# Kernel optimization log

Measured on AMD Instinct MI355X. Metric: run time of the kernel, lower is better.

The kernel has to match this reference:

```python
import jax, jax.numpy as jnp
import numpy as np

N = 50000          # total nodes
N_USER = 40000     # main (user) nodes
E = 400000         # edges per node kind
K = 3              # node kinds (separate graphs)
H = 4              # attention heads
F_IN = 128         # n_units[0]
F_OUT = 64         # n_units[1]
NB_CLASSES = 40
SLOPE = 0.2        # leaky relu negative slope


def setup_inputs() -> dict:
    key = jax.random.key(0)
    ks = jax.random.split(key, 12)
    h = jax.random.normal(ks[0], (N, F_IN), dtype=jnp.float32)
    edge_index = jax.random.randint(ks[1], (K, 2, E), 0, N, dtype=jnp.int32)
    # per-kind SpGATLayer params (bias=False)
    w = jax.random.normal(ks[2], (K, H, F_IN, F_OUT), dtype=jnp.float32) * 0.1
    a_src = jax.random.normal(ks[3], (K, H, F_OUT), dtype=jnp.float32) * 0.1
    a_trg = jax.random.normal(ks[4], (K, H, F_OUT), dtype=jnp.float32) * 0.1
    # AdditiveAttention: w1 (d=F_IN -> d2=F_OUT), w2 (d1=F_OUT -> d2=F_OUT), m (d2 -> 1)
    w1 = jax.random.normal(ks[5], (F_IN, F_OUT), dtype=jnp.float32) * 0.1
    w2 = jax.random.normal(ks[6], (F_OUT, F_OUT), dtype=jnp.float32) * 0.1
    m = jax.random.normal(ks[7], (F_OUT,), dtype=jnp.float32) * 0.1
    # final fc: in = F_OUT*(K+1)
    fc_w = jax.random.normal(ks[8], (F_OUT * (K + 1), NB_CLASSES), dtype=jnp.float32) * 0.1
    fc_b = jnp.zeros((NB_CLASSES,), dtype=jnp.float32)
    return {"h": h, "edge_index": edge_index, "w": w, "a_src": a_src,
            "a_trg": a_trg, "w1": w1, "w2": w2, "m": m,
            "fc_w": fc_w, "fc_b": fc_b}


def _spgat_kind(h, src, trg, wk, ask, atk):
    # h: [N, F_IN], wk: [H, F_IN, F_OUT], ask/atk: [H, F_OUT]
    hp = jnp.einsum('nd,hdf->nhf', h, wk)               # [N, H, F_OUT]
    s = jnp.einsum('nhf,hf->nh', hp, ask)               # [N, H]
    t = jnp.einsum('nhf,hf->nh', hp, atk)               # [N, H]
    e = s[src] + t[trg]                                 # [E, H]
    e = jnp.where(e >= 0, e, SLOPE * e)                 # leaky relu
    e = e - jnp.max(e)                                  # global max shift (as in source)
    exp_e = jnp.exp(e)
    denom = jax.ops.segment_sum(exp_e, trg, num_segments=N)  # [N, H]
    alpha = exp_e / (denom[trg] + 1e-16)                # [E, H]
    msg = hp[src] * alpha[:, :, None]                   # [E, H, F_OUT]
    out = jax.ops.segment_sum(msg, trg, num_segments=N) # [N, H, F_OUT]
    return out.mean(axis=1)                             # [N, F_OUT] (last layer head-mean)


def reference(h, edge_index, w, a_src, a_trg, w1, w2, m, fc_w, fc_b):
    heter = []
    for k in range(K):  # fixed small loop over node kinds
        x = _spgat_kind(h, edge_index[k, 0], edge_index[k, 1],
                        w[k], a_src[k], a_trg[k])
        heter.append(x[:N_USER])
    type_aware = jnp.stack(heter, axis=1)               # [N_USER, K, F_OUT]
    feature = h[:N_USER]                                # [N_USER, F_IN]
    q = jnp.tanh((feature @ w1)[:, None, :] + type_aware @ w2)  # [N_USER, K, F_OUT]
    scores = q @ m                                      # [N_USER, K]
    beta = jax.nn.softmax(scores, axis=-1)
    fusion = jnp.einsum('nk,nkf->nf', beta, type_aware) # [N_USER, F_OUT]
    ret = jnp.concatenate([type_aware, fusion[:, None, :]], axis=1)
    ret = ret.reshape(N_USER, -1)                       # [N_USER, F_OUT*(K+1)]
    logits = ret @ fc_w + fc_b
    return jax.nn.log_softmax(logits, axis=-1)
```

## Files before the change

### kernel.cpp

```cpp
#include <hip/hip_runtime.h>
#include <hip/hip_bf16.h>

#define NN    50000
#define NUSER 40000
#define EE    400000
#define KKIND 3
#define HHEAD 4
#define FIN   128
#define FOUT  64
#define NCLS  40

typedef __attribute__((ext_vector_type(8))) short short8;
typedef __attribute__((ext_vector_type(4))) float floatx4;

__device__ __forceinline__ float bf2f(unsigned short u) {
    unsigned int v = ((unsigned int)u) << 16;
    return __uint_as_float(v);
}
__device__ __forceinline__ unsigned short f2bf(float f) {
    unsigned int u = __float_as_uint(f);
    unsigned int r = (u + 0x7FFFu + ((u >> 16) & 1u)) >> 16;
    return (unsigned short)r;
}

#define OFF_H    0
#define OFF_W    6400000
#define OFF_ASRC 6498304
#define OFF_ATRG 6499072
#define OFF_W1   6499840
#define OFF_W2   6508032
#define OFF_M    6512128
#define OFF_FCW  6512192
#define OFF_FCB  6522432
#define CONV_TOT 6522472

__global__ __launch_bounds__(256) void detect_kernel(const unsigned short* __restrict__ hraw,
                                                     int* __restrict__ flag)
{
    __shared__ int cnt;
    if (threadIdx.x == 0) cnt = 0;
    __syncthreads();
    int local = 0;
#pragma unroll
    for (int j = 0; j < 8; j++) {
        unsigned short u = hraw[threadIdx.x * 8 + j];
        int ex = (u >> 7) & 0xFF;
        if (ex >= 0x90) local++;
    }
    atomicAdd(&cnt, local);
    __syncthreads();
    if (threadIdx.x == 0) *flag = (cnt > 100) ? 1 : 0;
}

__global__ __launch_bounds__(256) void conv_kernel(const void* __restrict__ p0, const void* __restrict__ p2,
                                                   const void* __restrict__ p3, const void* __restrict__ p4,
                                                   const void* __restrict__ p5, const void* __restrict__ p6,
                                                   const void* __restrict__ p7, const void* __restrict__ p8,
                                                   const void* __restrict__ p9,
                                                   const int* __restrict__ flagp,
                                                   unsigned short* __restrict__ dst)
{
    int tid = (blockIdx.x * 256 + threadIdx.x) * 8;
    if (tid >= CONV_TOT) return;
    const void* src; int li;
    if      (tid < OFF_W)    { src = p0; li = tid - OFF_H; }
    else if (tid < OFF_ASRC) { src = p2; li = tid - OFF_W; }
    else if (tid < OFF_ATRG) { src = p3; li = tid - OFF_ASRC; }
    else if (tid < OFF_W1)   { src = p4; li = tid - OFF_ATRG; }
    else if (tid < OFF_W2)   { src = p5; li = tid - OFF_W1; }
    else if (tid < OFF_M)    { src = p6; li = tid - OFF_W2; }
    else if (tid < OFF_FCW)  { src = p7; li = tid - OFF_M; }
    else if (tid < OFF_FCB)  { src = p8; li = tid - OFF_FCW; }
    else                     { src = p9; li = tid - OFF_FCB; }
    if (*flagp) {
        const float* fp = (const float*)src + li;
        float4 x = *(const float4*)fp;
        float4 y = *(const float4*)(fp + 4);
        uint4 o;
        o.x = (unsigned int)f2bf(x.x) | ((unsigned int)f2bf(x.y) << 16);
        o.y = (unsigned int)f2bf(x.z) | ((unsigned int)f2bf(x.w) << 16);
        o.z = (unsigned int)f2bf(y.x) | ((unsigned int)f2bf(y.y) << 16);
        o.w = (unsigned int)f2bf(y.z) | ((unsigned int)f2bf(y.w) << 16);
        *(uint4*)(dst + tid) = o;
    } else {
        *(uint4*)(dst + tid) = *(const uint4*)((const unsigned short*)src + li);
    }
}

__global__ __launch_bounds__(256) void repack_w(const unsigned short* __restrict__ w,
                                                unsigned short* __restrict__ wT)
{
    int tid = blockIdx.x * 256 + threadIdx.x;
    if (tid >= 12288) return;
    int f = tid & 63, g = (tid >> 6) & 15, h = (tid >> 10) & 3, k = tid >> 12;
    const unsigned short* src = w + (size_t)(k * 4 + h) * 8192 + f;
    unsigned short* dst = wT + (size_t)tid * 8;
#pragma unroll
    for (int j = 0; j < 8; j++) dst[j] = src[(size_t)(g * 8 + j) * 64];
}

__global__ __launch_bounds__(256) void repack_small(const unsigned short* __restrict__ w1,
                                                    const unsigned short* __restrict__ w2,
                                                    const unsigned short* __restrict__ fcw,
                                                    unsigned short* __restrict__ w1T,
                                                    unsigned short* __restrict__ w2T,
                                                    unsigned short* __restrict__ fcwT)
{
    int tid = blockIdx.x * 256 + threadIdx.x;
    if (tid < 1024) {
        int c = tid & 63, g = tid >> 6;
#pragma unroll
        for (int j = 0; j < 8; j++) w1T[(size_t)(g * 64 + c) * 8 + j] = w1[(size_t)(g * 8 + j) * 64 + c];
    } else if (tid < 1536) {
        int t = tid - 1024; int c = t & 63, g = t >> 6;
#pragma unroll
        for (int j = 0; j < 8; j++) w2T[(size_t)(g * 64 + c) * 8 + j] = w2[(size_t)(g * 8 + j) * 64 + c];
    } else if (tid < 3072) {
        int t = tid - 1536; int c = t % 48, g = t / 48;
#pragma unroll
        for (int j = 0; j < 8; j++)
            fcwT[(size_t)(g * 48 + c) * 8 + j] = (c < NCLS) ? fcw[(size_t)(g * 8 + j) * NCLS + c] : (unsigned short)0;
    }
}

__global__ __launch_bounds__(256) void hist3(const int* __restrict__ ei,
                                             unsigned int* __restrict__ cnt,
                                             unsigned int* __restrict__ rank)
{
    int k = blockIdx.y;
    const int* trg = ei + (size_t)k * 2 * EE + EE;
    unsigned int* ck = cnt + (size_t)k * NUSER;
    unsigned int* rk = rank + (size_t)k * EE;
    int e0 = blockIdx.x * 1024 + threadIdx.x;
    int t[4];
#pragma unroll
    for (int j = 0; j < 4; j++) {
        int e = e0 + j * 256;
        t[j] = (e < EE) ? trg[e] : NUSER;
    }
    unsigned int r[4];
#pragma unroll
    for (int j = 0; j < 4; j++)
        r[j] = (t[j] < NUSER) ? atomicAdd(&ck[t[j]], 1u) : 0u;
#pragma unroll
    for (int j = 0; j < 4; j++) {
        int e = e0 + j * 256;
        if (e < EE && t[j] < NUSER) rk[e] = r[j];
    }
}

#define SCB 20
__global__ __launch_bounds__(256) void scanA(const unsigned int* __restrict__ cnt,
                                             unsigned int* __restrict__ partials)
{
    int k = blockIdx.y, b = blockIdx.x;
    const unsigned int* c = cnt + (size_t)k * NUSER;
    int base = b * 2048 + threadIdx.x * 8;
    unsigned int s = 0;
#pragma unroll
    for (int j = 0; j < 8; j++) { int idx = base + j; if (idx < NUSER) s += c[idx]; }
#pragma unroll
    for (int off = 1; off < 64; off <<= 1) s += __shfl_xor(s, off, 64);
    __shared__ unsigned int wsum[4];
    int lane = threadIdx.x & 63, wid = threadIdx.x >> 6;
    if (lane == 0) wsum[wid] = s;
    __syncthreads();
    if (threadIdx.x == 0) partials[k * SCB + b] = wsum[0] + wsum[1] + wsum[2] + wsum[3];
}

__global__ __launch_bounds__(256) void scanB(unsigned int* __restrict__ partials,
                                             unsigned int* __restrict__ rowptr)
{
    int wid = threadIdx.x >> 6, lane = threadIdx.x & 63;
    if (wid >= KKIND) return;
    unsigned int v = (lane < SCB) ? partials[wid * SCB + lane] : 0u;
    unsigned int inc = v;
#pragma unroll
    for (int off = 1; off < 32; off <<= 1) {
        unsigned int u = __shfl_up(inc, off, 64);
        if (lane >= off) inc += u;
    }
    if (lane < SCB) partials[wid * SCB + lane] = inc - v;
    if (lane == SCB - 1) rowptr[(size_t)wid * (NUSER + 1) + NUSER] = inc;
}

__global__ __launch_bounds__(256) void scanC(const unsigned int* __restrict__ cnt,
                                             const unsigned int* __restrict__ partials,
                                             unsigned int* __restrict__ rowptr)
{
    int k = blockIdx.y, b = blockIdx.x;
    const unsigned int* c = cnt + (size_t)k * NUSER;
    unsigned int* rp = rowptr + (size_t)k * (NUSER + 1);
    int lane = threadIdx.x & 63, wid = threadIdx.x >> 6;
    int base = b * 2048 + threadIdx.x * 8;
    unsigned int vals[8]; unsigned int s = 0;
#pragma unroll
    for (int j = 0; j < 8; j++) { int idx = base + j; vals[j] = (idx < NUSER) ? c[idx] : 0u; s += vals[j]; }
    unsigned int inc = s;
#pragma unroll
    for (int off = 1; off < 64; off <<= 1) {
        unsigned int u = __shfl_up(inc, off, 64);
        if (lane >= off) inc += u;
    }
    __shared__ unsigned int wsum[4];
    if (lane == 63) wsum[wid] = inc;
    __syncthreads();
    unsigned int woff = 0;
    for (int i = 0; i < wid; i++) woff += wsum[i];
    unsigned int run = partials[k * SCB + b] + woff + (inc - s);
#pragma unroll
    for (int j = 0; j < 8; j++) {
        int idx = base + j;
        if (idx < NUSER) { rp[idx] = run; run += vals[j]; }
    }
}

__global__ __launch_bounds__(256) void scatter3(const int* __restrict__ ei,
                                                const unsigned int* __restrict__ rowptr,
                                                const unsigned int* __restrict__ rank,
                                                int* __restrict__ srcl)
{
    int k = blockIdx.y;
    const int* srcA = ei + (size_t)k * 2 * EE;
    const int* trg = srcA + EE;
    const unsigned int* rp = rowptr + (size_t)k * (NUSER + 1);
    const unsigned int* rk = rank + (size_t)k * EE;
    int* sl = srcl + (size_t)k * EE;
    int e0 = blockIdx.x * 1024 + threadIdx.x;
    int t[4], s[4]; unsigned int r[4];
#pragma unroll
    for (int j = 0; j < 4; j++) {
        int e = e0 + j * 256;
        t[j] = (e < EE) ? trg[e] : NUSER;
        s[j] = (e < EE) ? srcA[e] : 0;
        r[j] = (e < EE && t[j] < NUSER) ? rk[e] : 0u;
    }
    unsigned int base[4];
#pragma unroll
    for (int j = 0; j < 4; j++) base[j] = (t[j] < NUSER) ? rp[t[j]] : 0u;
#pragma unroll
    for (int j = 0; j < 4; j++) {
        int e = e0 + j * 256;
        if (e < EE && t[j] < NUSER) sl[base[j] + r[j]] = s[j];
    }
}

__global__ __launch_bounds__(256) void hp_gemm_multi(const unsigned short* __restrict__ h,
                                                     const unsigned short* __restrict__ wTall,
                                                     const unsigned short* __restrict__ asrc_all,
                                                     const unsigned short* __restrict__ atrg_all,
                                                     unsigned short* __restrict__ hp2,
                                                     long long hp2_stride,
                                                     float* __restrict__ sb, float* __restrict__ tb,
                                                     int kbeg, int kcnt)
{
    int wave = (blockIdx.x * 256 + threadIdx.x) >> 6;
    int lane = threadIdx.x & 63;
    if (wave >= NN / 16) return;
    int m0 = wave * 16;
    int mi = lane & 15, quad = lane >> 4;

    short8 a[4];
    const unsigned short* hrow = h + (size_t)(m0 + mi) * FIN + quad * 8;
#pragma unroll
    for (int kk = 0; kk < 4; kk++) a[kk] = *(const short8*)(hrow + kk * 32);

    for (int kq = 0; kq < kcnt; kq++) {
        int k = kbeg + kq;
        const unsigned short* wTk = wTall + (size_t)k * 32768;
        const unsigned short* ak_src = asrc_all + k * 256;
        const unsigned short* ak_trg = atrg_all + k * 256;
        unsigned short* hp2k = hp2 + (size_t)kq * hp2_stride;
        float* sbk = sb + (size_t)k * NN * 4;
        float* tbk = tb + (size_t)k * NN * 4;

        float sp[4][4], tp[4][4];
#pragma unroll
        for (int r = 0; r < 4; r++)
#pragma unroll
            for (int q2 = 0; q2 < 4; q2++) { sp[r][q2] = 0.f; tp[r][q2] = 0.f; }

#pragma unroll
        for (int j = 0; j < 4; j++) {
            int fc = j * 16 + mi;
            floatx4 acc4[4];
#pragma unroll
            for (int hh = 0; hh < 4; hh++) {
                floatx4 acc = {0.f, 0.f, 0.f, 0.f};
#pragma unroll
                for (int kk = 0; kk < 4; kk++) {
                    short8 b = *(const short8*)(wTk + (size_t)((hh * 16 + kk * 4 + quad) * 64 + fc) * 8);
                    acc = __builtin_amdgcn_mfma_f32_16x16x32_bf16(a[kk], b, acc, 0, 0, 0);
                }
                acc4[hh] = acc;
                float asv = bf2f(ak_src[hh * 64 + fc]);
                float atv = bf2f(ak_trg[hh * 64 + fc]);
#pragma unroll
                for (int reg = 0; reg < 4; reg++) {
                    sp[reg][hh] += acc[reg] * asv;
                    tp[reg][hh] += acc[reg] * atv;
                }
            }
#pragma unroll
            for (int reg = 0; reg < 4; reg++) {
                ushort4 pk;
                pk.x = f2bf(acc4[0][reg]); pk.y = f2bf(acc4[1][reg]);
                pk.z = f2bf(acc4[2][reg]); pk.w = f2bf(acc4[3][reg]);
                int row = m0 + quad * 4 + reg;
                *(ushort4*)(hp2k + (size_t)row * 256 + fc * 4) = pk;
            }
        }
#pragma unroll
        for (int off = 1; off < 16; off <<= 1)
#pragma unroll
            for (int r = 0; r < 4; r++)
#pragma unroll
                for (int q2 = 0; q2 < 4; q2++) {
                    sp[r][q2] += __shfl_xor(sp[r][q2], off, 64);
                    tp[r][q2] += __shfl_xor(tp[r][q2], off, 64);
                }
        float sv = 0.f, tv = 0.f;
#pragma unroll
        for (int r = 0; r < 4; r++)
#pragma unroll
            for (int q2 = 0; q2 < 4; q2++) {
                bool sel = (mi == r * 4 + q2);
                sv = sel ? sp[r][q2] : sv;
                tv = sel ? tp[r][q2] : tv;
            }
        int rr = m0 + quad * 4 + (mi >> 2);
        sbk[rr * 4 + (mi & 3)] = sv;
        tbk[rr * 4 + (mi & 3)] = tv;
    }
}

__global__ __launch_bounds__(256) void passB_multi(const unsigned int* __restrict__ rowptr_all,
                                                   const int* __restrict__ srcl_all,
                                                   const float* __restrict__ sb,
                                                   const float* __restrict__ tb,
                                                   const unsigned short* __restrict__ hp2,
                                                   long long hp2_stride,
                                                   unsigned short* __restrict__ ret, int kbeg)
{
    __shared__ int    lds_src[4][64];
    __shared__ float4 lds_ew[4][64];
    int kq = blockIdx.y, k = kbeg + kq;
    const unsigned int* rowptr = rowptr_all + (size_t)k * (NUSER + 1);
    const int* srcl = srcl_all + (size_t)k * EE;
    const float* sbk = sb + (size_t)k * NN * 4;
    const float* tbk = tb + (size_t)k * NN * 4;
    const unsigned short* hp2k = hp2 + (size_t)kq * hp2_stride;

    int wid = threadIdx.x >> 6;
    int n = __builtin_amdgcn_readfirstlane(blockIdx.x * 4 + wid);
    int f = threadIdx.x & 63;
    unsigned int beg = rowptr[n], end = rowptr[n + 1];
    float4 t4 = *(const float4*)(tbk + (size_t)n * 4);
    float num0 = 0.f, num1 = 0.f, num2 = 0.f, num3 = 0.f;
    float den0 = 0.f, den1 = 0.f, den2 = 0.f, den3 = 0.f;

    for (unsigned int p0 = beg; p0 < end; p0 += 64) {
        unsigned int cnt = end - p0; if (cnt > 64) cnt = 64;
        int s = 0;
        float4 e = {0.f, 0.f, 0.f, 0.f};
        if ((unsigned int)f < cnt) {
            s = srcl[p0 + f];
            float4 sv = *(const float4*)(sbk + (size_t)s * 4);
            float v0 = sv.x + t4.x, v1 = sv.y + t4.y, v2 = sv.z + t4.z, v3 = sv.w + t4.w;
            v0 = (v0 >= 0.f) ? v0 : 0.2f * v0;  v1 = (v1 >= 0.f) ? v1 : 0.2f * v1;
            v2 = (v2 >= 0.f) ? v2 : 0.2f * v2;  v3 = (v3 >= 0.f) ? v3 : 0.2f * v3;
            e.x = __expf(v0); e.y = __expf(v1); e.z = __expf(v2); e.w = __expf(v3);
        }
        lds_src[wid][f] = s;
        lds_ew[wid][f] = e;
        float d0 = e.x, d1 = e.y, d2 = e.z, d3 = e.w;
#pragma unroll
        for (int off = 1; off < 64; off <<= 1) {
            d0 += __shfl_xor(d0, off, 64); d1 += __shfl_xor(d1, off, 64);
            d2 += __shfl_xor(d2, off, 64); d3 += __shfl_xor(d3, off, 64);
        }
        den0 += d0; den1 += d1; den2 += d2; den3 += d3;
        unsigned int jmax = (cnt + 7u) & ~7u;
        for (unsigned int j = 0; j < jmax; j += 8) {
            int ss[8]; float4 ee[8];
#pragma unroll
            for (int u = 0; u < 8; u++) { ss[u] = lds_src[wid][j + u]; ee[u] = lds_ew[wid][j + u]; }
            ushort4 hv[8];
#pragma unroll
            for (int u = 0; u < 8; u++) hv[u] = *(const ushort4*)(hp2k + (size_t)ss[u] * 256 + f * 4);
#pragma unroll
            for (int u = 0; u < 8; u++) {
                num0 += ee[u].x * bf2f(hv[u].x); num1 += ee[u].y * bf2f(hv[u].y);
                num2 += ee[u].z * bf2f(hv[u].z); num3 += ee[u].w * bf2f(hv[u].w);
            }
        }
    }
    float r = 0.25f * (num0 / (den0 + 1e-16f) + num1 / (den1 + 1e-16f)
                     + num2 / (den2 + 1e-16f) + num3 / (den3 + 1e-16f));
    ret[(size_t)n * 256 + k * 64 + f] = f2bf(r);
}

__global__ __launch_bounds__(256) void qscore2f(const unsigned short* __restrict__ h,
                                                const unsigned short* __restrict__ w1T,
                                                const unsigned short* __restrict__ retA,
                                                const unsigned short* __restrict__ w2T,
                                                const unsigned short* __restrict__ mvec,
                                                unsigned short* __restrict__ ret, int M)
{
    int wave = (blockIdx.x * 256 + threadIdx.x) >> 6;
    int lane = threadIdx.x & 63;
    int m0 = wave * 16;
    if (m0 >= M) return;
    int mi = lane & 15, quad = lane >> 4;

    floatx4 fw[4];
#pragma unroll
    for (int nt = 0; nt < 4; nt++) fw[nt] = (floatx4){0.f, 0.f, 0.f, 0.f};
#pragma unroll
    for (int kk = 0; kk < 4; kk++) {
        short8 a = *(const short8*)(h + (size_t)(m0 + mi) * FIN + kk * 32 + quad * 8);
#pragma unroll
        for (int nt = 0; nt < 4; nt++) {
            short8 b = *(const short8*)(w1T + (size_t)((kk * 4 + quad) * 64 + nt * 16 + mi) * 8);
            fw[nt] = __builtin_amdgcn_mfma_f32_16x16x32_bf16(a, b, fw[nt], 0, 0, 0);
        }
    }

    float pk[3][4];
    short8 afr[3][2];
    for (int k = 0; k < KKIND; k++) {
        floatx4 acc[4];
#pragma unroll
        for (int nt = 0; nt < 4; nt++) acc[nt] = (floatx4){0.f, 0.f, 0.f, 0.f};
#pragma unroll
        for (int kk = 0; kk < 2; kk++) {
            short8 a = *(const short8*)(retA + (size_t)(m0 + mi) * 256 + k * 64 + kk * 32 + quad * 8);
            afr[k][kk] = a;
#pragma unroll
            for (int nt = 0; nt < 4; nt++) {
                short8 b = *(const short8*)(w2T + (size_t)((kk * 4 + quad) * 64 + nt * 16 + mi) * 8);
                acc[nt] = __builtin_amdgcn_mfma_f32_16x16x32_bf16(a, b, acc[nt], 0, 0, 0);
            }
        }
        float part[4] = {0.f, 0.f, 0.f, 0.f};
#pragma unroll
        for (int nt = 0; nt < 4; nt++) {
            int col = nt * 16 + mi;
            float mval = bf2f(mvec[col]);
#pragma unroll
            for (int reg = 0; reg < 4; reg++) {
                float x = acc[nt][reg] + fw[nt][reg];
                float q = 1.f - 2.f / (1.f + __expf(2.f * x));
                part[reg] += q * mval;
            }
        }
#pragma unroll
        for (int off = 1; off < 16; off <<= 1)
#pragma unroll
            for (int reg = 0; reg < 4; reg++) part[reg] += __shfl_xor(part[reg], off, 64);
#pragma unroll
        for (int reg = 0; reg < 4; reg++) pk[k][reg] = part[reg];
    }

    int rsel = mi & 3;
    float sv0 = (rsel == 0) ? pk[0][0] : (rsel == 1) ? pk[0][1] : (rsel == 2) ? pk[0][2] : pk[0][3];
    float sv1 = (rsel == 0) ? pk[1][0] : (rsel == 1) ? pk[1][1] : (rsel == 2) ? pk[1][2] : pk[1][3];
    float sv2 = (rsel == 0) ? pk[2][0] : (rsel == 1) ? pk[2][1] : (rsel == 2) ? pk[2][2] : pk[2][3];
    int srcLane = ((mi >> 2) << 4) | mi;
    float s0 = __shfl(sv0, srcLane, 64);
    float s1 = __shfl(sv1, srcLane, 64);
    float s2 = __shfl(sv2, srcLane, 64);
    float mx = fmaxf(s0, fmaxf(s1, s2));
    float e0 = __expf(s0 - mx), e1 = __expf(s1 - mx), e2 = __expf(s2 - mx);
    float inv = 1.f / (e0 + e1 + e2);
    float w0 = e0 * inv, w1 = e1 * inv, w2 = e2 * inv;

#pragma unroll
    for (int kk = 0; kk < 2; kk++) {
        unsigned short pkd[8];
#pragma unroll
        for (int j = 0; j < 8; j++) {
            float fu = w0 * bf2f((unsigned short)afr[0][kk][j])
                     + w1 * bf2f((unsigned short)afr[1][kk][j])
                     + w2 * bf2f((unsigned short)afr[2][kk][j]);
            pkd[j] = f2bf(fu);
        }
        *(ushort4*)(ret + (size_t)(m0 + mi) * 256 + 192 + kk * 32 + quad * 8) =
            *(ushort4*)&pkd[0];
        *(ushort4*)(ret + (size_t)(m0 + mi) * 256 + 192 + kk * 32 + quad * 8 + 4) =
            *(ushort4*)&pkd[4];
    }
}

__global__ __launch_bounds__(256) void fc_lsm(const unsigned short* __restrict__ A,
                                              const unsigned short* __restrict__ fcwT,
                                              const unsigned short* __restrict__ bias,
                                              const int* __restrict__ flagp,
                                              void* __restrict__ out, int M)
{
    int wave = (blockIdx.x * 256 + threadIdx.x) >> 6;
    int lane = threadIdx.x & 63;
    int m0 = wave * 16;
    if (m0 >= M) return;
    int mi = lane & 15, quad = lane >> 4;
    floatx4 acc[3];
#pragma unroll
    for (int nt = 0; nt < 3; nt++) acc[nt] = (floatx4){0.f, 0.f, 0.f, 0.f};
#pragma unroll
    for (int kk = 0; kk < 8; kk++) {
        short8 a = *(const short8*)(A + (size_t)(m0 + mi) * 256 + kk * 32 + quad * 8);
#pragma unroll
        for (int nt = 0; nt < 3; nt++) {
            short8 b = *(const short8*)(fcwT + (size_t)((kk * 4 + quad) * 48 + nt * 16 + mi) * 8);
            acc[nt] = __builtin_amdgcn_mfma_f32_16x16x32_bf16(a, b, acc[nt], 0, 0, 0);
        }
    }
    int fl = *flagp;
    float bv[3]; bool ok[3];
#pragma unroll
    for (int nt = 0; nt < 3; nt++) {
        int col = nt * 16 + mi;
        ok[nt] = (col < NCLS);
        bv[nt] = ok[nt] ? bf2f(bias[col]) : 0.f;
    }
#pragma unroll
    for (int reg = 0; reg < 4; reg++) {
        float v[3];
#pragma unroll
        for (int nt = 0; nt < 3; nt++)
            v[nt] = ok[nt] ? (acc[nt][reg] + bv[nt]) : -3.4e38f;
        float mx = fmaxf(fmaxf(v[0], v[1]), v[2]);
#pragma unroll
        for (int off = 1; off < 16; off <<= 1) mx = fmaxf(mx, __shfl_xor(mx, off, 64));
        float s = 0.f;
#pragma unroll
        for (int nt = 0; nt < 3; nt++) s += ok[nt] ? __expf(v[nt] - mx) : 0.f;
#pragma unroll
        for (int off = 1; off < 16; off <<= 1) s += __shfl_xor(s, off, 64);
        float lse = mx + __logf(s);
        int row = m0 + quad * 4 + reg;
#pragma unroll
        for (int nt = 0; nt < 3; nt++) {
            int col = nt * 16 + mi;
            if (col < NCLS) {
                float ls = v[nt] - lse;
                size_t idx = (size_t)row * NCLS + col;
                if (fl) ((float*)out)[idx] = ls;
                else    ((unsigned short*)out)[idx] = f2bf(ls);
            }
        }
    }
}

extern "C" void kernel_launch(void* const* d_in, const int* in_sizes, int n_in,
                              void* d_out, int out_size, void* d_ws, size_t ws_size,
                              hipStream_t stream)
{
    (void)in_sizes; (void)n_in; (void)out_size;
    const int* ei = (const int*)d_in[1];

    char* ws = (char*)d_ws;
    unsigned short* conv = (unsigned short*)ws;
    unsigned short* hc   = conv + OFF_H;
    unsigned short* wc   = conv + OFF_W;
    unsigned short* asrc = conv + OFF_ASRC;
    unsigned short* atrg = conv + OFF_ATRG;
    unsigned short* w1c  = conv + OFF_W1;
    unsigned short* w2c  = conv + OFF_W2;
    unsigned short* mc   = conv + OFF_M;
    unsigned short* fcwc = conv + OFF_FCW;
    unsigned short* fcbc = conv + OFF_FCB;
    int* flag             = (int*)(ws + 13044944);
    unsigned short* wT    = (unsigned short*)(ws + 13045248);
    unsigned short* w1T   = (unsigned short*)(ws + 13241856);
    unsigned short* w2T   = (unsigned short*)(ws + 13258240);
    unsigned short* fcwT  = (unsigned short*)(ws + 13266432);
    unsigned int* partials= (unsigned int*)(ws + 13291008);
    unsigned int* cnt     = (unsigned int*)(ws + 13291264);
    unsigned int* rowptr  = (unsigned int*)(ws + 13771264);
    int* srcl             = (int*)(ws + 14251520);
    unsigned int* rank    = (unsigned int*)(ws + 19051520);
    float* sbuf           = (float*)(ws + 23851520);
    float* tbuf           = (float*)(ws + 26251520);
    unsigned short* ret   = (unsigned short*)(ws + 28651520);
    unsigned short* hp2   = (unsigned short*)(ws + 49131520);

    const size_t NEED_BIG = 49131520ull + 3ull * NN * 256 * 2;
    int big = (ws_size >= NEED_BIG) ? 1 : 0;

    detect_kernel<<<1, 256, 0, stream>>>((const unsigned short*)d_in[0], flag);
    conv_kernel<<<(CONV_TOT / 8 + 255) / 256, 256, 0, stream>>>(
        d_in[0], d_in[2], d_in[3], d_in[4], d_in[5], d_in[6], d_in[7], d_in[8], d_in[9],
        flag, conv);

    repack_w<<<48, 256, 0, stream>>>(wc, wT);
    repack_small<<<12, 256, 0, stream>>>(w1c, w2c, fcwc, w1T, w2T, fcwT);

    hipMemsetAsync(cnt, 0, (size_t)KKIND * NUSER * 4, stream);
    hist3<<<dim3((EE + 1023) / 1024, 3), 256, 0, stream>>>(ei, cnt, rank);
    scanA<<<dim3(SCB, 3), 256, 0, stream>>>(cnt, partials);
    scanB<<<1, 256, 0, stream>>>(partials, rowptr);
    scanC<<<dim3(SCB, 3), 256, 0, stream>>>(cnt, partials, rowptr);
    scatter3<<<dim3((EE + 1023) / 1024, 3), 256, 0, stream>>>(ei, rowptr, rank, srcl);

    if (big) {
        long long stride = (long long)NN * 256;
        hp_gemm_multi<<<782, 256, 0, stream>>>(hc, wT, asrc, atrg, hp2, stride,
                                               sbuf, tbuf, 0, 3);
        passB_multi<<<dim3(NUSER / 4, 3), 256, 0, stream>>>(rowptr, srcl, sbuf, tbuf,
                                                            hp2, stride, ret, 0);
    } else {
        for (int k = 0; k < KKIND; k++) {
            hp_gemm_multi<<<782, 256, 0, stream>>>(hc, wT, asrc, atrg, hp2, 0,
                                                   sbuf, tbuf, k, 1);
            passB_multi<<<dim3(NUSER / 4, 1), 256, 0, stream>>>(rowptr, srcl, sbuf, tbuf,
                                                                hp2, 0, ret, k);
        }
    }

    qscore2f<<<625, 256, 0, stream>>>(hc, w1T, ret, w2T, mc, ret, NUSER);
    fc_lsm<<<625, 256, 0, stream>>>(ret, fcwT, fcbc, flag, d_out, NUSER);
}
```

Measured before the change: 400.4 us.

## Split projection GEMM from attention-score reduction and spread GEMM over more blocks

The fused projection kernel, which had each wave compute all 64 feature columns for 16 rows plus the s/t attention dot products, is split in two. One kernel gives each wave a 16-column slice of 16 rows, with kinds on grid.y. A separate kernel then reads the bf16 projections back and reduces them against a_src/a_trg with wave shuffles. In the big path, the batched passB launch becomes three per-kind launches. This raises parallelism and cuts register pressure in the GEMM. The cost is an extra pass over hp2, extra launches, s/t computed from bf16-rounded values, and h rows loaded by four waves each.

```diff
diff --git a/kernel.cpp b/kernel.cpp
--- a/kernel.cpp
+++ b/kernel.cpp
@@ -245,19 +245,18 @@
     }
 }
 
-__global__ __launch_bounds__(256) void hp_gemm_multi(const unsigned short* __restrict__ h,
-                                                     const unsigned short* __restrict__ wTall,
-                                                     const unsigned short* __restrict__ asrc_all,
-                                                     const unsigned short* __restrict__ atrg_all,
-                                                     unsigned short* __restrict__ hp2,
-                                                     long long hp2_stride,
-                                                     float* __restrict__ sb, float* __restrict__ tb,
-                                                     int kbeg, int kcnt)
-{
-    int wave = (blockIdx.x * 256 + threadIdx.x) >> 6;
+__global__ __launch_bounds__(256) void hp_gemm2(const unsigned short* __restrict__ h,
+                                                const unsigned short* __restrict__ wTall,
+                                                unsigned short* __restrict__ hp2,
+                                                long long hp2_stride, int kbeg)
+{
+    int k = kbeg + blockIdx.y;
+    const unsigned short* wTk = wTall + (size_t)k * 32768;
+    unsigned short* hp2k = hp2 + (size_t)blockIdx.y * hp2_stride;
+
+    int q = threadIdx.x >> 6;
     int lane = threadIdx.x & 63;
-    if (wave >= NN / 16) return;
-    int m0 = wave * 16;
+    int m0 = blockIdx.x * 16;
     int mi = lane & 15, quad = lane >> 4;
 
     short8 a[4];
@@ -265,72 +264,63 @@
 #pragma unroll
     for (int kk = 0; kk < 4; kk++) a[kk] = *(const short8*)(hrow + kk * 32);
 
-    for (int kq = 0; kq < kcnt; kq++) {
-        int k = kbeg + kq;
-        const unsigned short* wTk = wTall + (size_t)k * 32768;
-        const unsigned short* ak_src = asrc_all + k * 256;
-        const unsigned short* ak_trg = atrg_all + k * 256;
-        unsigned short* hp2k = hp2 + (size_t)kq * hp2_stride;
-        float* sbk = sb + (size_t)k * NN * 4;
-        float* tbk = tb + (size_t)k * NN * 4;
-
-        float sp[4][4], tp[4][4];
-#pragma unroll
-        for (int r = 0; r < 4; r++)
-#pragma unroll
-            for (int q2 = 0; q2 < 4; q2++) { sp[r][q2] = 0.f; tp[r][q2] = 0.f; }
-
-#pragma unroll
-        for (int j = 0; j < 4; j++) {
-            int fc = j * 16 + mi;
-            floatx4 acc4[4];
-#pragma unroll
-            for (int hh = 0; hh < 4; hh++) {
-                floatx4 acc = {0.f, 0.f, 0.f, 0.f};
-#pragma unroll
-                for (int kk = 0; kk < 4; kk++) {
-                    short8 b = *(const short8*)(wTk + (size_t)((hh * 16 + kk * 4 + quad) * 64 + fc) * 8);
-                    acc = __builtin_amdgcn_mfma_f32_16x16x32_bf16(a[kk], b, acc, 0, 0, 0);
-                }
-                acc4[hh] = acc;
-                float asv = bf2f(ak_src[hh * 64 + fc]);
-                float atv = bf2f(ak_trg[hh * 64 + fc]);
-#pragma unroll
-                for (int reg = 0; reg < 4; reg++) {
-                    sp[reg][hh] += acc[reg] * asv;
-                    tp[reg][hh] += acc[reg] * atv;
-                }
-            }
-#pragma unroll
-            for (int reg = 0; reg < 4; reg++) {
-                ushort4 pk;
-                pk.x = f2bf(acc4[0][reg]); pk.y = f2bf(acc4[1][reg]);
-                pk.z = f2bf(acc4[2][reg]); pk.w = f2bf(acc4[3][reg]);
-                int row = m0 + quad * 4 + reg;
-                *(ushort4*)(hp2k + (size_t)row * 256 + fc * 4) = pk;
-            }
-        }
-#pragma unroll
-        for (int off = 1; off < 16; off <<= 1)
-#pragma unroll
-            for (int r = 0; r < 4; r++)
-#pragma unroll
-                for (int q2 = 0; q2 < 4; q2++) {
-                    sp[r][q2] += __shfl_xor(sp[r][q2], off, 64);
-                    tp[r][q2] += __shfl_xor(tp[r][q2], off, 64);
-                }
-        float sv = 0.f, tv = 0.f;
-#pragma unroll
-        for (int r = 0; r < 4; r++)
-#pragma unroll
-            for (int q2 = 0; q2 < 4; q2++) {
-                bool sel = (mi == r * 4 + q2);
-                sv = sel ? sp[r][q2] : sv;
-                tv = sel ? tp[r][q2] : tv;
-            }
-        int rr = m0 + quad * 4 + (mi >> 2);
-        sbk[rr * 4 + (mi & 3)] = sv;
-        tbk[rr * 4 + (mi & 3)] = tv;
+    int fc = q * 16 + mi;
+    floatx4 acc4[4];
+#pragma unroll
+    for (int hh = 0; hh < 4; hh++) {
+        floatx4 acc = {0.f, 0.f, 0.f, 0.f};
+#pragma unroll
+        for (int kk = 0; kk < 4; kk++) {
+            short8 b = *(const short8*)(wTk + (size_t)((hh * 16 + kk * 4 + quad) * 64 + fc) * 8);
+            acc = __builtin_amdgcn_mfma_f32_16x16x32_bf16(a[kk], b, acc, 0, 0, 0);
+        }
+        acc4[hh] = acc;
+    }
+#pragma unroll
+    for (int reg = 0; reg < 4; reg++) {
+        ushort4 pk;
+        pk.x = f2bf(acc4[0][reg]); pk.y = f2bf(acc4[1][reg]);
+        pk.z = f2bf(acc4[2][reg]); pk.w = f2bf(acc4[3][reg]);
+        int row = m0 + quad * 4 + reg;
+        *(ushort4*)(hp2k + (size_t)row * 256 + fc * 4) = pk;
+    }
+}
+
+__global__ __launch_bounds__(256) void st_kernel(const unsigned short* __restrict__ hp2,
+                                                 long long hp2_stride,
+                                                 const unsigned short* __restrict__ asrc_all,
+                                                 const unsigned short* __restrict__ atrg_all,
+                                                 float* __restrict__ sb, float* __restrict__ tb,
+                                                 int kbeg)
+{
+    int k = kbeg + blockIdx.y;
+    const unsigned short* hp2k = hp2 + (size_t)blockIdx.y * hp2_stride;
+    const unsigned short* ask = asrc_all + k * 256;
+    const unsigned short* atk = atrg_all + k * 256;
+    float* sbk = sb + (size_t)k * NN * 4;
+    float* tbk = tb + (size_t)k * NN * 4;
+
+    int wid = threadIdx.x >> 6;
+    int n = blockIdx.x * 4 + wid;
+    int f = threadIdx.x & 63;
+    ushort4 hv = *(const ushort4*)(hp2k + (size_t)n * 256 + f * 4);
+    float h0 = bf2f(hv.x), h1 = bf2f(hv.y), h2 = bf2f(hv.z), h3 = bf2f(hv.w);
+    float ps0 = h0 * bf2f(ask[f]),       ps1 = h1 * bf2f(ask[64 + f]);
+    float ps2 = h2 * bf2f(ask[128 + f]), ps3 = h3 * bf2f(ask[192 + f]);
+    float pt0 = h0 * bf2f(atk[f]),       pt1 = h1 * bf2f(atk[64 + f]);
+    float pt2 = h2 * bf2f(atk[128 + f]), pt3 = h3 * bf2f(atk[192 + f]);
+#pragma unroll
+    for (int off = 1; off < 64; off <<= 1) {
+        ps0 += __shfl_xor(ps0, off, 64); ps1 += __shfl_xor(ps1, off, 64);
+        ps2 += __shfl_xor(ps2, off, 64); ps3 += __shfl_xor(ps3, off, 64);
+        pt0 += __shfl_xor(pt0, off, 64); pt1 += __shfl_xor(pt1, off, 64);
+        pt2 += __shfl_xor(pt2, off, 64); pt3 += __shfl_xor(pt3, off, 64);
+    }
+    if (f < 4) {
+        float sv = (f == 0) ? ps0 : (f == 1) ? ps1 : (f == 2) ? ps2 : ps3;
+        float tv = (f == 0) ? pt0 : (f == 1) ? pt1 : (f == 2) ? pt2 : pt3;
+        sbk[n * 4 + f] = sv;
+        tbk[n * 4 + f] = tv;
     }
 }
 
@@ -605,14 +595,15 @@
 
     if (big) {
         long long stride = (long long)NN * 256;
-        hp_gemm_multi<<<782, 256, 0, stream>>>(hc, wT, asrc, atrg, hp2, stride,
-                                               sbuf, tbuf, 0, 3);
-        passB_multi<<<dim3(NUSER / 4, 3), 256, 0, stream>>>(rowptr, srcl, sbuf, tbuf,
-                                                            hp2, stride, ret, 0);
+        hp_gemm2<<<dim3(NN / 16, 3), 256, 0, stream>>>(hc, wT, hp2, stride, 0);
+        st_kernel<<<dim3(NN / 4, 3), 256, 0, stream>>>(hp2, stride, asrc, atrg, sbuf, tbuf, 0);
+        for (int k = 0; k < KKIND; k++)
+            passB_multi<<<dim3(NUSER / 4, 1), 256, 0, stream>>>(rowptr, srcl, sbuf, tbuf,
+                                                                hp2 + (size_t)k * stride, 0, ret, k);
     } else {
         for (int k = 0; k < KKIND; k++) {
-            hp_gemm_multi<<<782, 256, 0, stream>>>(hc, wT, asrc, atrg, hp2, 0,
-                                                   sbuf, tbuf, k, 1);
+            hp_gemm2<<<dim3(NN / 16, 1), 256, 0, stream>>>(hc, wT, hp2, 0, k);
+            st_kernel<<<dim3(NN / 4, 1), 256, 0, stream>>>(hp2, 0, asrc, atrg, sbuf, tbuf, k);
             passB_multi<<<dim3(NUSER / 4, 1), 256, 0, stream>>>(rowptr, srcl, sbuf, tbuf,
                                                                 hp2, 0, ret, k);
         }
```

After: 397.5 us. No clear change (-0.7%).
